# Kernel tuning notes

Hardware: AMD Instinct MI355X
Metric: run time of the kernel (lower is better)

The kernel has to match this reference:

```python
import jax, jax.numpy as jnp
import numpy as np

N_NODES = 32768
N_GRAPHS = 16
N_PER = N_NODES // N_GRAPHS  # 2048 nodes per graph
N_EDGES = 262144
D = 128      # node_state_dim
DE = 64      # edge_state_dim
H = 256      # edge hidden / message dim (= 2*D, required by matching prop)
NH = 256     # node MLP hidden


def _mlp2(x, W1, b1, W2, b2):
    # Linear -> ReLU -> Linear (torch nn.Linear convention: y = x @ W.T + b)
    return jax.nn.relu(x @ W1.T + b1) @ W2.T + b2


def setup_inputs() -> dict:
    key = jax.random.key(0)
    ks = jax.random.split(key, 16)
    s = 0.1  # edge_net_init_scale-ish small init
    inp = {
        "node_states": jax.random.normal(ks[0], (N_NODES, D), jnp.float32),
        "edge_features": jax.random.normal(ks[1], (N_EDGES, DE), jnp.float32),
        "from_idx": jax.random.randint(ks[2], (N_EDGES,), 0, N_NODES, jnp.int32),
        "to_idx": jax.random.randint(ks[3], (N_EDGES,), 0, N_NODES, jnp.int32),
        "graph_idx": jnp.repeat(jnp.arange(N_GRAPHS, dtype=jnp.int32), N_PER),
        "n_graphs": N_GRAPHS,
        # forward message net: Linear(2D+DE -> H), Linear(H -> H)
        "Wm1": jax.random.normal(ks[4], (H, 2 * D + DE), jnp.float32) * s,
        "bm1": jnp.zeros((H,), jnp.float32),
        "Wm2": jax.random.normal(ks[5], (H, H), jnp.float32) * s,
        "bm2": jnp.zeros((H,), jnp.float32),
        # reverse message net (separate params)
        "Wr1": jax.random.normal(ks[6], (H, 2 * D + DE), jnp.float32) * s,
        "br1": jnp.zeros((H,), jnp.float32),
        "Wr2": jax.random.normal(ks[7], (H, H), jnp.float32) * s,
        "br2": jnp.zeros((H,), jnp.float32),
        # node update MLP: Linear(4D -> NH), Linear(NH -> D)
        "Wn1": jax.random.normal(ks[8], (NH, 4 * D), jnp.float32) * s,
        "bn1": jnp.zeros((NH,), jnp.float32),
        "Wn2": jax.random.normal(ks[9], (D, NH), jnp.float32) * s,
        "bn2": jnp.zeros((D,), jnp.float32),
    }
    return inp


def _forward(node_states, edge_features, from_idx, to_idx, n_graphs,
             Wm1, bm1, Wm2, bm2, Wr1, br1, Wr2, br2, Wn1, bn1, Wn2, bn2):
    n = node_states.shape[0]
    fs = node_states[from_idx]   # [E, D] gather
    ts = node_states[to_idx]     # [E, D]
    # forward direction: messages -> scatter-add into to_idx
    m_fwd = _mlp2(jnp.concatenate([fs, ts, edge_features], -1), Wm1, bm1, Wm2, bm2)
    agg = jax.ops.segment_sum(m_fwd, to_idx, num_segments=n)
    # reverse direction: swap endpoints, scatter-add into from_idx
    m_rev = _mlp2(jnp.concatenate([ts, fs, edge_features], -1), Wr1, br1, Wr2, br2)
    agg = agg + jax.ops.segment_sum(m_rev, from_idx, num_segments=n)

    # cross-graph dual-softmax attention over (i, i+1) graph pairs.
    # graph_idx is contiguous equal-size blocks -> reshape partitioning.
    n_per = n // n_graphs
    d = node_states.reshape(n_graphs // 2, 2, n_per, -1)
    x, y = d[:, 0], d[:, 1]                      # [P, Np, D] each
    a = jnp.einsum('pid,pjd->pij', x, y)         # dotproduct similarity
    a_x = jax.nn.softmax(a, axis=2)              # softmax over y per x-row
    a_y = jax.nn.softmax(a, axis=1)              # softmax over x per y-col
    attn_x = jnp.einsum('pij,pjd->pid', a_x, y)  # [P, Np, D]
    attn_y = jnp.einsum('pij,pid->pjd', a_y, x)  # [P, Np, D]
    cross = jnp.stack([attn_x, attn_y], axis=1).reshape(n, -1)

    attention_input = node_states - cross
    node_inputs = jnp.concatenate([agg, attention_input, node_states], -1)  # [N, 4D]
    mlp_out = _mlp2(node_inputs, Wn1, bn1, Wn2, bn2)
    return node_states + mlp_out  # residual update


def reference(node_states, edge_features, from_idx, to_idx, graph_idx, n_graphs,
              Wm1, bm1, Wm2, bm2, Wr1, br1, Wr2, br2, Wn1, bn1, Wn2, bn2):
    return _forward(node_states, edge_features, from_idx, to_idx, int(n_graphs),
                    Wm1, bm1, Wm2, bm2, Wr1, br1, Wr2, br2, Wn1, bn1, Wn2, bn2)
```

## Files before the change

kernel.cpp:

```cpp
#include <hip/hip_runtime.h>


typedef __bf16 bf16_t;
typedef __bf16 bf16x8 __attribute__((ext_vector_type(8)));
typedef __bf16 bf16x4 __attribute__((ext_vector_type(4)));
typedef float  f32x4  __attribute__((ext_vector_type(4)));

#define MFMA16(a,b,c) __builtin_amdgcn_mfma_f32_16x16x32_bf16((a),(b),(c),0,0,0)

constexpr int NNODES = 32768;
constexpr int NEDGES = 262144;
constexpr int DD = 128;
constexpr int HH = 256;

__device__ __forceinline__ bf16x8 cvt8(f32x4 a, f32x4 b){
  bf16x8 r;
  r[0]=(bf16_t)a[0]; r[1]=(bf16_t)a[1]; r[2]=(bf16_t)a[2]; r[3]=(bf16_t)a[3];
  r[4]=(bf16_t)b[0]; r[5]=(bf16_t)b[1]; r[6]=(bf16_t)b[2]; r[7]=(bf16_t)b[3];
  return r;
}

__global__ void cvt_wp_kernel(const float* __restrict__ Wm1, const float* __restrict__ Wr1,
                              bf16_t* __restrict__ wp){
  int idx = (blockIdx.x*256 + threadIdx.x)*4;
  int n = idx >> 7, k = idx & 127;
  const float* W = (n < 512) ? Wm1 : Wr1;
  int row = n & 255;
  int colbase = ((n >> 8) & 1) * 128;
  f32x4 v = *(const f32x4*)(W + (size_t)row*320 + colbase + k);
  bf16x4 o; o[0]=(bf16_t)v[0]; o[1]=(bf16_t)v[1]; o[2]=(bf16_t)v[2]; o[3]=(bf16_t)v[3];
  *(bf16x4*)(wp + idx) = o;
}

__global__ void pack_wc_kernel(const float* __restrict__ Wm1, const float* __restrict__ Wr1,
                               bf16_t* __restrict__ wc){
  int g = blockIdx.x*256 + threadIdx.x;
  int part = g >> 11, gg = g & 2047;
  int tile = gg >> 6, lane = gg & 63;
  int kc = tile >> 4, nt = tile & 15;
  int lr = lane & 15, lk = lane >> 4;
  const float* W = part ? Wr1 : Wm1;
  int row = nt*16 + lr;
  int col = 256 + kc*32 + lk*8;
  f32x4 v0 = *(const f32x4*)(W + (size_t)row*320 + col);
  f32x4 v1 = *(const f32x4*)(W + (size_t)row*320 + col + 4);
  *(bf16x8*)(wc + (size_t)g*8) = cvt8(v0,v1);
}

__global__ void pack_wn2_kernel(const float* __restrict__ Wn2, bf16_t* __restrict__ out){
  int g = blockIdx.x*256 + threadIdx.x;
  int tile = g >> 6, lane = g & 63;
  int kc = tile >> 3, nt = tile & 7;
  int lr = lane & 15, lk = lane >> 4;
  int row = nt*16 + lr;
  int col = kc*32 + lk*8;
  f32x4 v0 = *(const f32x4*)(Wn2 + (size_t)row*256 + col);
  f32x4 v1 = *(const f32x4*)(Wn2 + (size_t)row*256 + col + 4);
  *(bf16x8*)(out + (size_t)g*8) = cvt8(v0,v1);
}

__global__ void hist_kernel(const int* __restrict__ to_idx, const int* __restrict__ from_idx,
                            int* __restrict__ cnt_to, int* __restrict__ cnt_from){
  int e = blockIdx.x*256 + threadIdx.x;
  if (e < NEDGES){
    atomicAdd(&cnt_to[to_idx[e]], 1);
    atomicAdd(&cnt_from[from_idx[e]], 1);
  }
}

__global__ void scan_kernel(int* __restrict__ cnt, int* __restrict__ start){
  __shared__ int sums[1024];
  const int t = threadIdx.x;
  int local[32]; int s = 0;
  #pragma unroll
  for (int j=0;j<32;j++){ local[j] = cnt[t*32+j]; s += local[j]; }
  sums[t] = s; __syncthreads();
  #pragma unroll
  for (int d=1; d<1024; d<<=1){
    int v = (t>=d) ? sums[t-d] : 0;
    __syncthreads();
    sums[t] += v;
    __syncthreads();
  }
  int off = sums[t] - s;
  #pragma unroll
  for (int j=0;j<32;j++){
    start[t*32+j] = off;
    cnt[t*32+j]   = off;
    off += local[j];
  }
  if (t == 1023) start[32768] = sums[1023];
}

__global__ void place_kernel(const int* __restrict__ to_idx, const int* __restrict__ from_idx,
                             int* __restrict__ cur_to, int* __restrict__ cur_from,
                             int* __restrict__ eid_to, int* __restrict__ eid_from,
                             int* __restrict__ rowv_to, int* __restrict__ rowv_from){
  int e = blockIdx.x*256 + threadIdx.x;
  if (e < NEDGES){
    int vt = to_idx[e];
    int p = atomicAdd(&cur_to[vt], 1);
    eid_to[p] = e;
    rowv_to[p] = vt;
    int vf = from_idx[e];
    int q = atomicAdd(&cur_from[vf], 1);
    eid_from[q] = e;
    rowv_from[q] = vf;
  }
}

__global__ __launch_bounds__(256,3) void proj_kernel(
    const float* __restrict__ ns, const bf16_t* __restrict__ Wp,
    bf16_t* __restrict__ P1, bf16_t* __restrict__ P2)
{
  constexpr int XS = 136;
  constexpr int CS = 264;
  __shared__ bf16_t Xs[64*XS];
  __shared__ bf16_t Cs[64*CS];
  const int tid = threadIdx.x;
  const int rb = blockIdx.x*64;
  const int cb = blockIdx.y;
  #pragma unroll
  for (int it=0; it<8; ++it){
    int c = tid + it*256;
    int row = c >> 5, co = (c & 31)*4;
    f32x4 v = *(const f32x4*)(ns + (size_t)(rb+row)*DD + co);
    bf16x4 o; o[0]=(bf16_t)v[0]; o[1]=(bf16_t)v[1]; o[2]=(bf16_t)v[2]; o[3]=(bf16_t)v[3];
    *(bf16x4*)&Xs[row*XS + co] = o;
  }
  __syncthreads();
  const int lane = tid & 63, wave = tid >> 6, lr = lane & 15, lk = lane >> 4;
  const bf16_t* Wb = Wp + (size_t)cb*256*128;
  f32x4 acc[16];
  #pragma unroll
  for (int nt=0;nt<16;nt++) acc[nt] = (f32x4){0.f,0.f,0.f,0.f};
  #pragma unroll
  for (int kc=0;kc<4;kc++){
    bf16x8 a = *(const bf16x8*)&Xs[(wave*16 + lr)*XS + kc*32 + lk*8];
    #pragma unroll
    for (int nt=0;nt<16;nt++){
      bf16x8 b = *(const bf16x8*)&Wb[(size_t)(nt*16 + lr)*128 + kc*32 + lk*8];
      acc[nt] = MFMA16(a,b,acc[nt]);
    }
  }
  #pragma unroll
  for (int nt=0;nt<16;nt++)
    #pragma unroll
    for (int r=0;r<4;r++)
      Cs[(wave*16 + lk*4 + r)*CS + nt*16 + lr] = (bf16_t)acc[nt][r];
  __syncthreads();
  bf16_t* P = cb ? P2 : P1;
  #pragma unroll
  for (int it=0; it<8; ++it){
    int c = tid + it*256;
    int row = c >> 5, co = (c & 31)*8;
    *(bf16x8*)&P[(size_t)(rb+row)*HH + co] = *(const bf16x8*)&Cs[row*CS + co];
  }
}

__global__ __launch_bounds__(256,4) void edge_agg_kernel(
    const float* __restrict__ ef, const bf16_t* __restrict__ Wc,
    const int* __restrict__ eid, const int* __restrict__ oth,
    const int* __restrict__ rowv, const int* __restrict__ start,
    const bf16_t* __restrict__ P1, const bf16_t* __restrict__ P2,
    const float* __restrict__ b1,
    float* __restrict__ partial, bf16_t* __restrict__ aggh)
{
  constexpr int CS = 264;
  __shared__ bf16_t Cs[64*CS];
  __shared__ int es[64], os[64], vs[64];
  const int tid = threadIdx.x;
  const int rb = blockIdx.x*64;
  if (tid < 64){
    int e = eid[rb + tid];
    es[tid] = e;
    os[tid] = oth[e];
    vs[tid] = rowv[rb + tid];
  }
  __syncthreads();

  const int lane = tid & 63, wave = tid >> 6, lr = lane & 15, lk = lane >> 4;
  {
    const float* arow = ef + (size_t)es[wave*16 + lr]*64;
    bf16x8 a0, a1;
    {
      f32x4 v0 = *(const f32x4*)(arow + lk*8);
      f32x4 v1 = *(const f32x4*)(arow + lk*8 + 4);
      a0 = cvt8(v0,v1);
      f32x4 w0 = *(const f32x4*)(arow + 32 + lk*8);
      f32x4 w1 = *(const f32x4*)(arow + 32 + lk*8 + 4);
      a1 = cvt8(w0,w1);
    }
    #pragma unroll
    for (int p=0;p<2;p++){
      f32x4 acc[8];
      #pragma unroll
      for (int nt=0;nt<8;nt++) acc[nt] = (f32x4){0.f,0.f,0.f,0.f};
      #pragma unroll
      for (int nt=0;nt<8;nt++){
        bf16x8 b0 = *(const bf16x8*)&Wc[(size_t)((0*16 + p*8 + nt)*64 + lane)*8];
        acc[nt] = MFMA16(a0,b0,acc[nt]);
        bf16x8 b1v = *(const bf16x8*)&Wc[(size_t)((1*16 + p*8 + nt)*64 + lane)*8];
        acc[nt] = MFMA16(a1,b1v,acc[nt]);
      }
      #pragma unroll
      for (int nt=0;nt<8;nt++)
        #pragma unroll
        for (int r=0;r<4;r++)
          Cs[(wave*16 + lk*4 + r)*CS + (p*8+nt)*16 + lr] = (bf16_t)acc[nt][r];
    }
  }
  __syncthreads();

  const int c8 = (tid & 31) * 8;
  const int rbase = (tid >> 5) * 8;
  {
    f32x4 b1a = *(const f32x4*)(b1 + c8);
    f32x4 b1b = *(const f32x4*)(b1 + c8 + 4);
    #pragma unroll
    for (int j=0;j<8;j++){
      const int row = rbase + j;
      bf16x8 cs = *(const bf16x8*)&Cs[row*CS + c8];
      bf16x8 p1 = *(const bf16x8*)&P1[(size_t)os[row]*HH + c8];
      bf16x8 p2 = *(const bf16x8*)&P2[(size_t)vs[row]*HH + c8];
      bf16x8 o;
      #pragma unroll
      for (int k=0;k<4;k++){
        o[k]   = (bf16_t)fmaxf((float)cs[k]   + (float)p1[k]   + (float)p2[k]   + b1a[k], 0.f);
        o[4+k] = (bf16_t)fmaxf((float)cs[4+k] + (float)p1[4+k] + (float)p2[4+k] + b1b[k], 0.f);
      }
      *(bf16x8*)&Cs[row*CS + c8] = o;
    }
  }
  __syncthreads();

  const int c = tid;
  float runsum = 0.f;
  int curv = vs[0];
  for (int row=0; row<64; ++row){
    const int v = vs[row];
    if (v != curv){
      const int s0 = start[curv], s1 = start[curv+1];
      if (s0 >= rb && s1 <= rb+64)
        aggh[(size_t)curv*HH + c] = (bf16_t)runsum;
      else
        partial[((size_t)curv*2 + (s0 >= rb ? 0 : 1))*HH + c] = runsum;
      runsum = 0.f; curv = v;
    }
    runsum += (float)Cs[row*CS + c];
  }
  {
    const int s0 = start[curv], s1 = start[curv+1];
    if (s0 >= rb && s1 <= rb+64)
      aggh[(size_t)curv*HH + c] = (bf16_t)runsum;
    else
      partial[((size_t)curv*2 + (s0 >= rb ? 0 : 1))*HH + c] = runsum;
  }
}

__global__ __launch_bounds__(256) void combine_kernel(
    const float* __restrict__ partial, const int* __restrict__ start,
    bf16_t* __restrict__ aggh)
{
  const int tid = threadIdx.x;
  const int v = blockIdx.x*8 + (tid>>5);
  const int c0 = (tid & 31)*8;
  const int s0 = start[v], s1 = start[v+1];
  if (s1 == s0){
    bf16x8 z;
    #pragma unroll
    for (int j=0;j<8;j++) z[j] = (bf16_t)0.f;
    *(bf16x8*)&aggh[(size_t)v*HH + c0] = z;
  } else if ((s0>>6) != ((s1-1)>>6)){
    const float* p0 = partial + ((size_t)v*2    )*HH + c0;
    const float* p1 = partial + ((size_t)v*2 + 1)*HH + c0;
    f32x4 a0 = *(const f32x4*)p0;
    f32x4 a1 = *(const f32x4*)(p0+4);
    f32x4 c1 = *(const f32x4*)p1;
    f32x4 c2 = *(const f32x4*)(p1+4);
    bf16x8 o;
    #pragma unroll
    for (int j=0;j<4;j++){ o[j]=(bf16_t)(a0[j]+c1[j]); o[4+j]=(bf16_t)(a1[j]+c2[j]); }
    *(bf16x8*)&aggh[(size_t)v*HH + c0] = o;
  }
}

__global__ __launch_bounds__(256) void w2t_kernel(const float* __restrict__ Wm2, const float* __restrict__ Wr2,
                                                  bf16_t* __restrict__ wm2T, bf16_t* __restrict__ wr2T){
  __shared__ bf16_t t[64][72];
  const int bi = (blockIdx.x & 3)*64;
  const int bj = ((blockIdx.x>>2) & 3)*64;
  const int m  = blockIdx.x >> 4;
  const float* W = m ? Wr2 : Wm2;
  bf16_t* WT = m ? wr2T : wm2T;
  const int tid = threadIdx.x;
  #pragma unroll
  for (int it=0; it<16; ++it){
    int c = tid + it*256;
    int r = c >> 6, co = c & 63;
    t[r][co] = (bf16_t)W[(size_t)(bi+r)*256 + bj + co];
  }
  __syncthreads();
  #pragma unroll
  for (int it=0; it<16; ++it){
    int c = tid + it*256;
    int r = c >> 6, co = c & 63;
    WT[(size_t)(bj+r)*256 + bi + co] = t[co][r];
  }
}

__global__ __launch_bounds__(256,2) void wcat_gemm_kernel(
    const float* __restrict__ Wn1, const bf16_t* __restrict__ wm2T, const bf16_t* __restrict__ wr2T,
    bf16_t* __restrict__ wcat)
{
  constexpr int XS = 264, CS = 264;
  __shared__ bf16_t Xs[64*XS];
  __shared__ bf16_t Cs[64*CS];
  const int tid = threadIdx.x;
  const int rb = blockIdx.x*64;
  const int cb = blockIdx.y;
  const bf16_t* BT = cb ? wr2T : wm2T;
  #pragma unroll
  for (int it=0; it<16; ++it){
    int c = tid + it*256;
    int row = c >> 6, co = (c & 63)*4;
    f32x4 v = *(const f32x4*)(Wn1 + (size_t)(rb+row)*512 + co);
    bf16x4 o; o[0]=(bf16_t)v[0]; o[1]=(bf16_t)v[1]; o[2]=(bf16_t)v[2]; o[3]=(bf16_t)v[3];
    *(bf16x4*)&Xs[row*XS + co] = o;
  }
  __syncthreads();
  const int lane = tid & 63, wave = tid >> 6, lr = lane & 15, lk = lane >> 4;
  f32x4 acc[16];
  #pragma unroll
  for (int nt=0;nt<16;nt++) acc[nt] = (f32x4){0.f,0.f,0.f,0.f};
  #pragma unroll
  for (int kc=0;kc<8;kc++){
    bf16x8 a = *(const bf16x8*)&Xs[(wave*16 + lr)*XS + kc*32 + lk*8];
    #pragma unroll
    for (int nt=0;nt<16;nt++){
      bf16x8 b = *(const bf16x8*)&BT[(size_t)(nt*16 + lr)*256 + kc*32 + lk*8];
      acc[nt] = MFMA16(a,b,acc[nt]);
    }
  }
  #pragma unroll
  for (int nt=0;nt<16;nt++)
    #pragma unroll
    for (int r=0;r<4;r++)
      Cs[(wave*16 + lk*4 + r)*CS + nt*16 + lr] = (bf16_t)acc[nt][r];
  __syncthreads();
  const int nt_base = rb >> 4;
  #pragma unroll
  for (int it=0; it<8; ++it){
    int g = tid + it*256;
    int tile = g >> 6, lane2 = g & 63;
    int kc_l = tile >> 2, nt_l = tile & 3;
    int lr2 = lane2 & 15, lk2 = lane2 >> 4;
    bf16x8 v = *(const bf16x8*)&Cs[(nt_l*16 + lr2)*CS + kc_l*32 + lk2*8];
    *(bf16x8*)&wcat[(size_t)(((cb*8 + kc_l)*16 + nt_base + nt_l)*64 + lane2)*8] = v;
  }
}

__global__ void wcat_copy_kernel(const float* __restrict__ Wn1, bf16_t* __restrict__ wcat){
  int g = blockIdx.x*256 + threadIdx.x;
  int tile = g >> 6, lane = g & 63;
  int kc = tile >> 4, nt = tile & 15;
  int lr = lane & 15, lk = lane >> 4;
  int row = nt*16 + lr;
  int col = 256 + kc*32 + lk*8;
  f32x4 v0 = *(const f32x4*)(Wn1 + (size_t)row*512 + col);
  f32x4 v1 = *(const f32x4*)(Wn1 + (size_t)row*512 + col + 4);
  *(bf16x8*)&wcat[(size_t)(((16 + kc)*16 + nt)*64 + lane)*8] = cvt8(v0,v1);
}

__global__ __launch_bounds__(256) void uw_kernel(const float* __restrict__ Wn1,
    const float* __restrict__ bm2, const float* __restrict__ br2,
    float* __restrict__ u, float* __restrict__ w){
  const int n = threadIdx.x;
  float su=0.f, sw=0.f;
  for (int j=0;j<256;j+=4){
    f32x4 wv = *(const f32x4*)(Wn1 + (size_t)n*512 + j);
    f32x4 bu = *(const f32x4*)(bm2 + j);
    f32x4 bw = *(const f32x4*)(br2 + j);
    #pragma unroll
    for (int q=0;q<4;q++){ su += wv[q]*bu[q]; sw += wv[q]*bw[q]; }
  }
  u[n]=su; w[n]=sw;
}

__global__ __launch_bounds__(256) void nst_kernel(const float* __restrict__ ns,
                                                  bf16_t* __restrict__ nsT,
                                                  bf16_t* __restrict__ nsB){
  constexpr int XS2 = 136;
  __shared__ bf16_t Xs[64*XS2];
  const int tid = threadIdx.x;
  const int nb = blockIdx.x*64;
  #pragma unroll
  for (int it=0; it<8; ++it){
    int c = tid + it*256;
    int rowl = c >> 5, co = (c & 31)*4;
    f32x4 v = *(const f32x4*)(ns + (size_t)(nb+rowl)*DD + co);
    bf16x4 o; o[0]=(bf16_t)v[0]; o[1]=(bf16_t)v[1]; o[2]=(bf16_t)v[2]; o[3]=(bf16_t)v[3];
    *(bf16x4*)&Xs[rowl*XS2 + co] = o;
    *(bf16x4*)&nsB[(size_t)(nb+rowl)*DD + co] = o;
  }
  __syncthreads();
  const int sb = nb >> 11;
  const int jb = nb & 2047;
  bf16_t* outp = nsT + (size_t)sb*DD*2048 + jb;
  #pragma unroll
  for (int it=0; it<4; ++it){
    int c = tid + it*256;
    int d = c >> 3, g8 = (c & 7)*8;
    bf16x8 o;
    #pragma unroll
    for (int k=0;k<8;k++){
      int s64 = g8 + k;
      int t32 = s64 >> 5, s = s64 & 31;
      int m = (s & 1) ? (16 + (s>>1)) : (s>>1);
      o[k] = Xs[(t32*32 + m)*XS2 + d];
    }
    *(bf16x8*)(outp + (size_t)d*2048 + g8) = o;
  }
}

__global__ __launch_bounds__(256,3) void attn_kernel(
    const bf16_t* __restrict__ nsB, const bf16_t* __restrict__ nsT,
    float* __restrict__ Opart, float* __restrict__ lpart)
{
  constexpr int KS = 136;
  constexpr int VS = 40;
  constexpr int PS = 40;
  __shared__ bf16_t Ks[2][32*KS];
  __shared__ bf16_t Vt[2][128*VS];
  __shared__ bf16_t Ps[64*PS];
  const int tid = threadIdx.x;
  const int lane = tid & 63, wave = tid >> 6, lr = lane & 15, lk = lane >> 4;
  const int bx = blockIdx.x;
  const int qt = bx & 31, side = (bx>>5)&1, p = (bx>>6)&7, kvh = bx>>9;
  const size_t qbase = (size_t)p*4096 + (size_t)side*2048 + (size_t)qt*64;
  const int sbkv = p*2 + (side^1);
  const bf16_t* Kv = nsB + ((size_t)p*4096 + (size_t)(side^1)*2048)*DD + (size_t)kvh*32*32*DD;
  const bf16_t* Vp = nsT + (size_t)sbkv*DD*2048 + (size_t)kvh*32*32;

  bf16x8 qf[4];
  {
    const bf16_t* qrow = nsB + (qbase + wave*16 + lr)*DD;
    #pragma unroll
    for (int kc=0;kc<4;kc++) qf[kc] = *(const bf16x8*)(qrow + kc*32 + lk*8);
  }
  float ls[4] = {0.f,0.f,0.f,0.f};
  f32x4 acco[8];
  #pragma unroll
  for (int nt=0;nt<8;nt++) acco[nt]=(f32x4){0.f,0.f,0.f,0.f};

  const int krow0 = tid>>4,        kcol = (tid&15)*8;
  const int vd0   = tid>>2,        vsl  = (tid&3)*8;
  bf16x8 kreg0, kreg1, vreg0, vreg1;

  auto load_tile = [&](int t){
    const bf16_t* kp = Kv + (size_t)t*32*DD;
    kreg0 = *(const bf16x8*)(kp + (size_t)krow0*DD + kcol);
    kreg1 = *(const bf16x8*)(kp + (size_t)(krow0+16)*DD + kcol);
    const bf16_t* vp = Vp + t*32;
    vreg0 = *(const bf16x8*)(vp + (size_t)vd0*2048 + vsl);
    vreg1 = *(const bf16x8*)(vp + (size_t)(vd0+64)*2048 + vsl);
  };
  auto store_tile = [&](int b){
    *(bf16x8*)&Ks[b][krow0*KS + kcol]      = kreg0;
    *(bf16x8*)&Ks[b][(krow0+16)*KS + kcol] = kreg1;
    *(bf16x8*)&Vt[b][vd0*VS + vsl]         = vreg0;
    *(bf16x8*)&Vt[b][(vd0+64)*VS + vsl]    = vreg1;
  };

  load_tile(0);
  store_tile(0);
  load_tile(1);
  __syncthreads();
  int cur = 0;
  for (int t=0; t<32; ++t){
    if (t+1 < 32){
      store_tile(cur^1);
      if (t+2 < 32) load_tile(t+2);
    }
    f32x4 s0 = (f32x4){0.f,0.f,0.f,0.f}, s1 = (f32x4){0.f,0.f,0.f,0.f};
    #pragma unroll
    for (int kc=0;kc<4;kc++){
      bf16x8 b0 = *(const bf16x8*)&Ks[cur][lr*KS      + kc*32 + lk*8];
      bf16x8 b1 = *(const bf16x8*)&Ks[cur][(16+lr)*KS + kc*32 + lk*8];
      s0 = MFMA16(qf[kc], b0, s0);
      s1 = MFMA16(qf[kc], b1, s1);
    }
    #pragma unroll
    for (int r=0;r<4;r++){
      float p0 = __expf(s0[r] - 40.f);
      float p1 = __expf(s1[r] - 40.f);
      ls[r] += p0 + p1;
      union { bf16_t h[2]; unsigned u; } pk;
      pk.h[0] = (bf16_t)p0; pk.h[1] = (bf16_t)p1;
      *(unsigned*)&Ps[(wave*16 + lk*4 + r)*PS + 2*lr] = pk.u;
    }
    asm volatile("s_waitcnt lgkmcnt(0)" ::: "memory");
    __builtin_amdgcn_sched_barrier(0);
    bf16x8 pa = *(const bf16x8*)&Ps[(wave*16 + lr)*PS + lk*8];
    #pragma unroll
    for (int nt=0;nt<8;nt++){
      bf16x8 vb = *(const bf16x8*)&Vt[cur][(nt*16+lr)*VS + lk*8];
      acco[nt] = MFMA16(pa, vb, acco[nt]);
    }
    __syncthreads();
    cur ^= 1;
  }
  #pragma unroll
  for (int r=0;r<4;r++){
    float v = ls[r];
    v += __shfl_xor(v,1); v += __shfl_xor(v,2);
    v += __shfl_xor(v,4); v += __shfl_xor(v,8);
    ls[r] = v;
  }
  float* Op = Opart + (size_t)kvh*NNODES*DD;
  #pragma unroll
  for (int r=0;r<4;r++){
    const size_t row = qbase + wave*16 + lk*4 + r;
    if (lr == 0) lpart[(size_t)kvh*NNODES + row] = ls[r];
    #pragma unroll
    for (int nt=0;nt<8;nt++)
      Op[row*DD + nt*16 + lr] = acco[nt][r];
  }
}

__global__ __launch_bounds__(256) void attn_combine_kernel(
    const float* __restrict__ ns, const float* __restrict__ Opart,
    const float* __restrict__ lpart, bf16_t* __restrict__ attnB)
{
  const int tid = threadIdx.x;
  const int row = blockIdx.x*16 + (tid >> 4);
  const int c0 = (tid & 15)*8;
  const float inv = 1.f/(lpart[row] + lpart[NNODES + row]);
  const float* o0 = Opart + (size_t)row*DD + c0;
  const float* o1 = Opart + (size_t)NNODES*DD + (size_t)row*DD + c0;
  const float* nr = ns + (size_t)row*DD + c0;
  f32x4 a0 = *(const f32x4*)o0,      a1 = *(const f32x4*)(o0+4);
  f32x4 b0 = *(const f32x4*)o1,      b1 = *(const f32x4*)(o1+4);
  f32x4 n0 = *(const f32x4*)nr,      n1 = *(const f32x4*)(nr+4);
  bf16x8 o;
  #pragma unroll
  for (int j=0;j<4;j++){
    o[j]   = (bf16_t)(n0[j] - (a0[j]+b0[j])*inv);
    o[4+j] = (bf16_t)(n1[j] - (a1[j]+b1[j])*inv);
  }
  *(bf16x8*)&attnB[(size_t)row*DD + c0] = o;
}

__global__ __launch_bounds__(256,2) void node_mlp_kernel(
    const bf16_t* __restrict__ agghf, const bf16_t* __restrict__ agghr,
    const bf16_t* __restrict__ attnB, const bf16_t* __restrict__ nsB,
    const float* __restrict__ ns,
    const bf16_t* __restrict__ wcat, const float* __restrict__ bn1,
    const float* __restrict__ uvec, const float* __restrict__ wvec,
    const int* __restrict__ start_to, const int* __restrict__ start_from,
    const bf16_t* __restrict__ Wn2b, const float* __restrict__ bn2,
    float* __restrict__ out)
{
  __shared__ __align__(16) bf16_t As[32*768];
  bf16_t* Hs = As;
  const int tid = threadIdx.x;
  const int lane = tid & 63, wave = tid >> 6, lr = lane & 15, lk = lane >> 4;
  const int rb = blockIdx.x*32;

  bf16x8 stg[12];
  int dsta[12];
  #pragma unroll
  for (int it=0; it<12; ++it){
    const int db = it*4096 + tid*16;
    const int row = db / 1536;
    const int within = db - row*1536;
    const size_t node = (size_t)(rb + row);
    const char* s0 = (const char*)agghf + (node<<9) + within;
    const char* s1 = (const char*)agghr + (node<<9) + (within-512);
    const char* s2 = (const char*)attnB + (node<<8) + (within-1024);
    const char* s3 = (const char*)nsB   + (node<<8) + (within-1280);
    const char* src = within < 512 ? s0 : (within < 1024 ? s1 : (within < 1280 ? s2 : s3));
    stg[it] = *(const bf16x8*)src;
    dsta[it] = row*1536 + (within ^ ((row & 7) << 4));
  }
  #pragma unroll
  for (int it=0; it<12; ++it)
    *(bf16x8*)((char*)As + dsta[it]) = stg[it];
  __syncthreads();

  const int cg = wave >> 1;
  const int colbase = cg * 128;
  const int arow = (wave & 1)*16 + lr;
  const unsigned abase = (unsigned)arow * 1536u;
  const unsigned asw = ((unsigned)(arow & 7)) << 4;
  f32x4 acc[8];
  #pragma unroll
  for (int nt=0;nt<8;nt++) acc[nt] = (f32x4){0.f,0.f,0.f,0.f};
  #pragma unroll
  for (int kc=0; kc<24; ++kc){
    const unsigned y = (unsigned)(kc*64 + lk*16);
    bf16x8 a = *(const bf16x8*)((const char*)As + abase + (y ^ asw));
    #pragma unroll
    for (int nt=0;nt<8;nt++){
      bf16x8 b = *(const bf16x8*)&wcat[(size_t)((kc*16 + cg*8 + nt)*64 + lane)*8];
      acc[nt] = MFMA16(a,b,acc[nt]);
    }
  }
  __syncthreads();

  const int r0 = rb + (wave&1)*16 + lk*4;
  float dt[4], df[4];
  #pragma unroll
  for (int r=0;r<4;r++){
    dt[r] = (float)(start_to[r0+r+1]   - start_to[r0+r]);
    df[r] = (float)(start_from[r0+r+1] - start_from[r0+r]);
  }
  #pragma unroll
  for (int nt=0;nt<8;nt++){
    const int col = colbase + nt*16 + lr;
    const float bias = bn1[col];
    const float uu = uvec[col], ww = wvec[col];
    #pragma unroll
    for (int r=0;r<4;r++){
      float v = acc[nt][r] + bias + dt[r]*uu + df[r]*ww;
      v = v > 0.f ? v : 0.f;
      Hs[((wave&1)*16 + lk*4 + r)*264 + col] = (bf16_t)v;
    }
  }
  __syncthreads();

  const int cb2 = cg * 64;
  f32x4 acc2[4];
  #pragma unroll
  for (int nt=0;nt<4;nt++) acc2[nt] = (f32x4){0.f,0.f,0.f,0.f};
  #pragma unroll
  for (int kc=0;kc<8;kc++){
    bf16x8 a = *(const bf16x8*)&Hs[((wave&1)*16 + lr)*264 + kc*32 + lk*8];
    #pragma unroll
    for (int nt=0;nt<4;nt++){
      bf16x8 b = *(const bf16x8*)&Wn2b[(size_t)((kc*8 + cg*4 + nt)*64 + lane)*8];
      acc2[nt] = MFMA16(a,b,acc2[nt]);
    }
  }
  #pragma unroll
  for (int nt=0;nt<4;nt++){
    const int col = cb2 + nt*16 + lr;
    const float bias = bn2[col];
    #pragma unroll
    for (int r=0;r<4;r++){
      const size_t rr = (size_t)(r0 + r);
      out[rr*DD + col] = acc2[nt][r] + bias + ns[rr*DD + col];
    }
  }
}

extern "C" void kernel_launch(void* const* d_in, const int* in_sizes, int n_in,
                              void* d_out, int out_size, void* d_ws, size_t ws_size,
                              hipStream_t stream) {
  const float* ns  = (const float*)d_in[0];
  const float* ef  = (const float*)d_in[1];
  const int* from_idx = (const int*)d_in[2];
  const int* to_idx   = (const int*)d_in[3];
  const float* Wm1 = (const float*)d_in[6];  const float* bm1 = (const float*)d_in[7];
  const float* Wm2 = (const float*)d_in[8];  const float* bm2 = (const float*)d_in[9];
  const float* Wr1 = (const float*)d_in[10]; const float* br1 = (const float*)d_in[11];
  const float* Wr2 = (const float*)d_in[12]; const float* br2 = (const float*)d_in[13];
  const float* Wn1 = (const float*)d_in[14]; const float* bn1 = (const float*)d_in[15];
  const float* Wn2 = (const float*)d_in[16]; const float* bn2 = (const float*)d_in[17];

  char* ws = (char*)d_ws;
  float*  partial  = (float*)(ws);
  int*    rowv_to   = (int*)(ws + 67108864);
  int*    rowv_from = (int*)(ws + 68157440);
  bf16_t* P1t    = (bf16_t*)(ws + 134217728);
  bf16_t* P2t    = (bf16_t*)(ws + 150994944);
  bf16_t* aggh_f = (bf16_t*)(ws + 167772160);
  bf16_t* aggh_r = (bf16_t*)(ws + 184549376);
  bf16_t* wpb  = (bf16_t*)(ws + 201326592);
  bf16_t* wcb  = (bf16_t*)(ws + 201588736);
  bf16_t* wn2b = (bf16_t*)(ws + 201654272);
  int* cur_to     = (int*)(ws + 202244096);
  int* cur_from   = (int*)(ws + 202375168);
  int* start_to   = (int*)(ws + 202506240);
  int* start_from = (int*)(ws + 202637320);
  int* eid_to     = (int*)(ws + 202768400);
  int* eid_from   = (int*)(ws + 203816976);
  bf16_t* attnB = (bf16_t*)(ws);
  bf16_t* nsB   = (bf16_t*)(ws + 33554432);
  bf16_t* nsT   = (bf16_t*)(ws + 41943040);
  bf16_t* wm2T  = (bf16_t*)(ws + 50331648);
  bf16_t* wr2T  = (bf16_t*)(ws + 50462720);
  bf16_t* wcat  = (bf16_t*)(ws + 50593792);
  float*  uvec  = (float*) (ws + 50987008);
  float*  wvec  = (float*) (ws + 50988032);
  float*  Opart = (float*) (ws + 69206016);
  float*  lpart = (float*) (ws + 102760448);

  hipMemsetAsync(cur_to, 0, 2*NNODES*sizeof(int), stream);

  cvt_wp_kernel<<<128, 256, 0, stream>>>(Wm1, Wr1, wpb);
  pack_wc_kernel<<<16, 256, 0, stream>>>(Wm1, Wr1, wcb);
  pack_wn2_kernel<<<16, 256, 0, stream>>>(Wn2, wn2b);

  hist_kernel<<<NEDGES/256, 256, 0, stream>>>(to_idx, from_idx, cur_to, cur_from);
  scan_kernel<<<1, 1024, 0, stream>>>(cur_to, start_to);
  scan_kernel<<<1, 1024, 0, stream>>>(cur_from, start_from);
  place_kernel<<<NEDGES/256, 256, 0, stream>>>(to_idx, from_idx, cur_to, cur_from,
      eid_to, eid_from, rowv_to, rowv_from);

  proj_kernel<<<dim3(NNODES/64, 2), 256, 0, stream>>>(ns, wpb, P1t, P2t);
  edge_agg_kernel<<<NEDGES/64, 256, 0, stream>>>(ef, wcb, eid_to, from_idx,
      rowv_to, start_to, P1t, P2t, bm1, partial, aggh_f);
  combine_kernel<<<NNODES/8, 256, 0, stream>>>(partial, start_to, aggh_f);

  proj_kernel<<<dim3(NNODES/64, 2), 256, 0, stream>>>(ns, wpb + 512*128, P1t, P2t);
  edge_agg_kernel<<<NEDGES/64, 256, 0, stream>>>(ef, wcb + 256*64, eid_from, to_idx,
      rowv_from, start_from, P1t, P2t, br1, partial, aggh_r);
  combine_kernel<<<NNODES/8, 256, 0, stream>>>(partial, start_from, aggh_r);

  nst_kernel<<<NNODES/64, 256, 0, stream>>>(ns, nsT, nsB);
  w2t_kernel<<<32, 256, 0, stream>>>(Wm2, Wr2, wm2T, wr2T);
  wcat_gemm_kernel<<<dim3(4,2), 256, 0, stream>>>(Wn1, wm2T, wr2T, wcat);
  wcat_copy_kernel<<<32, 256, 0, stream>>>(Wn1, wcat);
  uw_kernel<<<1, 256, 0, stream>>>(Wn1, bm2, br2, uvec, wvec);

  attn_kernel<<<1024, 256, 0, stream>>>(nsB, nsT, Opart, lpart);
  attn_combine_kernel<<<NNODES/16, 256, 0, stream>>>(ns, Opart, lpart, attnB);

  node_mlp_kernel<<<NNODES/32, 256, 0, stream>>>(aggh_f, aggh_r, attnB, nsB, ns,
      wcat, bn1, uvec, wvec, start_to, start_from, wn2b, bn2, (float*)d_out);
}
```

Before: 452.8 us.

## Merge forward/reverse edge passes and fuse small prep kernels into fewer launches

Fuses the three weight-pack kernels, the two scans, the two directions of proj/edge_agg/combine, and the w2t/uw/wcat_copy kernels into single launches using block-index dispatch. It also moves the first-layer bias into the P2 projection and stores split-segment partials in bf16 instead of fp32. The goals are fewer kernel launches, more concurrent blocks for the edge work, and less partial-sum traffic. The cost is extra workspace for separate forward and reverse P buffers, plus a small precision loss from the bf16 partials and the earlier bias rounding.

```diff
diff --git a/kernel.cpp b/kernel.cpp
--- a/kernel.cpp
+++ b/kernel.cpp
@@ -20,43 +20,44 @@
   return r;
 }
 
-__global__ void cvt_wp_kernel(const float* __restrict__ Wm1, const float* __restrict__ Wr1,
-                              bf16_t* __restrict__ wp){
-  int idx = (blockIdx.x*256 + threadIdx.x)*4;
-  int n = idx >> 7, k = idx & 127;
-  const float* W = (n < 512) ? Wm1 : Wr1;
-  int row = n & 255;
-  int colbase = ((n >> 8) & 1) * 128;
-  f32x4 v = *(const f32x4*)(W + (size_t)row*320 + colbase + k);
-  bf16x4 o; o[0]=(bf16_t)v[0]; o[1]=(bf16_t)v[1]; o[2]=(bf16_t)v[2]; o[3]=(bf16_t)v[3];
-  *(bf16x4*)(wp + idx) = o;
-}
-
-__global__ void pack_wc_kernel(const float* __restrict__ Wm1, const float* __restrict__ Wr1,
-                               bf16_t* __restrict__ wc){
-  int g = blockIdx.x*256 + threadIdx.x;
-  int part = g >> 11, gg = g & 2047;
-  int tile = gg >> 6, lane = gg & 63;
-  int kc = tile >> 4, nt = tile & 15;
-  int lr = lane & 15, lk = lane >> 4;
-  const float* W = part ? Wr1 : Wm1;
-  int row = nt*16 + lr;
-  int col = 256 + kc*32 + lk*8;
-  f32x4 v0 = *(const f32x4*)(W + (size_t)row*320 + col);
-  f32x4 v1 = *(const f32x4*)(W + (size_t)row*320 + col + 4);
-  *(bf16x8*)(wc + (size_t)g*8) = cvt8(v0,v1);
-}
-
-__global__ void pack_wn2_kernel(const float* __restrict__ Wn2, bf16_t* __restrict__ out){
-  int g = blockIdx.x*256 + threadIdx.x;
-  int tile = g >> 6, lane = g & 63;
-  int kc = tile >> 3, nt = tile & 7;
-  int lr = lane & 15, lk = lane >> 4;
-  int row = nt*16 + lr;
-  int col = kc*32 + lk*8;
-  f32x4 v0 = *(const f32x4*)(Wn2 + (size_t)row*256 + col);
-  f32x4 v1 = *(const f32x4*)(Wn2 + (size_t)row*256 + col + 4);
-  *(bf16x8*)(out + (size_t)g*8) = cvt8(v0,v1);
+__global__ void pack_weights_kernel(const float* __restrict__ Wm1, const float* __restrict__ Wr1,
+                                    const float* __restrict__ Wn2,
+                                    bf16_t* __restrict__ wp, bf16_t* __restrict__ wc,
+                                    bf16_t* __restrict__ wn2){
+  const int bx = blockIdx.x;
+  const int tid = threadIdx.x;
+  if (bx < 128){
+    int idx = (bx*256 + tid)*4;
+    int n = idx >> 7, k = idx & 127;
+    const float* W = (n < 512) ? Wm1 : Wr1;
+    int row = n & 255;
+    int colbase = ((n >> 8) & 1) * 128;
+    f32x4 v = *(const f32x4*)(W + (size_t)row*320 + colbase + k);
+    bf16x4 o; o[0]=(bf16_t)v[0]; o[1]=(bf16_t)v[1]; o[2]=(bf16_t)v[2]; o[3]=(bf16_t)v[3];
+    *(bf16x4*)(wp + idx) = o;
+  } else if (bx < 144){
+    int g = (bx-128)*256 + tid;
+    int part = g >> 11, gg = g & 2047;
+    int tile = gg >> 6, lane = gg & 63;
+    int kc = tile >> 4, nt = tile & 15;
+    int lr = lane & 15, lk = lane >> 4;
+    const float* W = part ? Wr1 : Wm1;
+    int row = nt*16 + lr;
+    int col = 256 + kc*32 + lk*8;
+    f32x4 v0 = *(const f32x4*)(W + (size_t)row*320 + col);
+    f32x4 v1 = *(const f32x4*)(W + (size_t)row*320 + col + 4);
+    *(bf16x8*)(wc + (size_t)g*8) = cvt8(v0,v1);
+  } else {
+    int g = (bx-144)*256 + tid;
+    int tile = g >> 6, lane = g & 63;
+    int kc = tile >> 3, nt = tile & 7;
+    int lr = lane & 15, lk = lane >> 4;
+    int row = nt*16 + lr;
+    int col = kc*32 + lk*8;
+    f32x4 v0 = *(const f32x4*)(Wn2 + (size_t)row*256 + col);
+    f32x4 v1 = *(const f32x4*)(Wn2 + (size_t)row*256 + col + 4);
+    *(bf16x8*)(wn2 + (size_t)g*8) = cvt8(v0,v1);
+  }
 }
 
 __global__ void hist_kernel(const int* __restrict__ to_idx, const int* __restrict__ from_idx,
@@ -68,7 +69,10 @@
   }
 }
 
-__global__ void scan_kernel(int* __restrict__ cnt, int* __restrict__ start){
+__global__ void scan_kernel(int* __restrict__ cnt_to, int* __restrict__ cnt_from,
+                            int* __restrict__ start_to, int* __restrict__ start_from){
+  int* cnt   = blockIdx.x ? cnt_from : cnt_to;
+  int* start = blockIdx.x ? start_from : start_to;
   __shared__ int sums[1024];
   const int t = threadIdx.x;
   int local[32]; int s = 0;
@@ -111,7 +115,9 @@
 
 __global__ __launch_bounds__(256,3) void proj_kernel(
     const float* __restrict__ ns, const bf16_t* __restrict__ Wp,
-    bf16_t* __restrict__ P1, bf16_t* __restrict__ P2)
+    const float* __restrict__ bm1, const float* __restrict__ br1,
+    bf16_t* __restrict__ P1f, bf16_t* __restrict__ P2f,
+    bf16_t* __restrict__ P1r, bf16_t* __restrict__ P2r)
 {
   constexpr int XS = 136;
   constexpr int CS = 264;
@@ -120,6 +126,8 @@
   const int tid = threadIdx.x;
   const int rb = blockIdx.x*64;
   const int cb = blockIdx.y;
+  const int dir = blockIdx.z;
+  const float* bvec = dir ? br1 : bm1;
   #pragma unroll
   for (int it=0; it<8; ++it){
     int c = tid + it*256;
@@ -130,7 +138,7 @@
   }
   __syncthreads();
   const int lane = tid & 63, wave = tid >> 6, lr = lane & 15, lk = lane >> 4;
-  const bf16_t* Wb = Wp + (size_t)cb*256*128;
+  const bf16_t* Wb = Wp + (size_t)(dir*2 + cb)*32768;
   f32x4 acc[16];
   #pragma unroll
   for (int nt=0;nt<16;nt++) acc[nt] = (f32x4){0.f,0.f,0.f,0.f};
@@ -144,12 +152,14 @@
     }
   }
   #pragma unroll
-  for (int nt=0;nt<16;nt++)
+  for (int nt=0;nt<16;nt++){
+    const float bias = cb ? bvec[nt*16 + lr] : 0.f;
     #pragma unroll
     for (int r=0;r<4;r++)
-      Cs[(wave*16 + lk*4 + r)*CS + nt*16 + lr] = (bf16_t)acc[nt][r];
-  __syncthreads();
-  bf16_t* P = cb ? P2 : P1;
+      Cs[(wave*16 + lk*4 + r)*CS + nt*16 + lr] = (bf16_t)(acc[nt][r] + bias);
+  }
+  __syncthreads();
+  bf16_t* P = dir ? (cb ? P2r : P1r) : (cb ? P2f : P1f);
   #pragma unroll
   for (int it=0; it<8; ++it){
     int c = tid + it*256;
@@ -160,17 +170,31 @@
 
 __global__ __launch_bounds__(256,4) void edge_agg_kernel(
     const float* __restrict__ ef, const bf16_t* __restrict__ Wc,
-    const int* __restrict__ eid, const int* __restrict__ oth,
-    const int* __restrict__ rowv, const int* __restrict__ start,
-    const bf16_t* __restrict__ P1, const bf16_t* __restrict__ P2,
-    const float* __restrict__ b1,
-    float* __restrict__ partial, bf16_t* __restrict__ aggh)
+    const int* __restrict__ eid_to, const int* __restrict__ eid_from,
+    const int* __restrict__ from_idx, const int* __restrict__ to_idx,
+    const int* __restrict__ rowv_to, const int* __restrict__ rowv_from,
+    const int* __restrict__ start_to, const int* __restrict__ start_from,
+    const bf16_t* __restrict__ P1f, const bf16_t* __restrict__ P2f,
+    const bf16_t* __restrict__ P1r, const bf16_t* __restrict__ P2r,
+    bf16_t* __restrict__ partial_f, bf16_t* __restrict__ partial_r,
+    bf16_t* __restrict__ aggh_f, bf16_t* __restrict__ aggh_r)
 {
   constexpr int CS = 264;
   __shared__ bf16_t Cs[64*CS];
   __shared__ int es[64], os[64], vs[64];
   const int tid = threadIdx.x;
-  const int rb = blockIdx.x*64;
+  const int dir = blockIdx.x >> 12;
+  const int rb = (blockIdx.x & 4095)*64;
+  const int* eid  = dir ? eid_from  : eid_to;
+  const int* oth  = dir ? to_idx    : from_idx;
+  const int* rowv = dir ? rowv_from : rowv_to;
+  const int* start= dir ? start_from: start_to;
+  const bf16_t* P1 = dir ? P1r : P1f;
+  const bf16_t* P2 = dir ? P2r : P2f;
+  bf16_t* partial  = dir ? partial_r : partial_f;
+  bf16_t* aggh     = dir ? aggh_r : aggh_f;
+  const bf16_t* Wcd = Wc + (size_t)dir*16384;
+
   if (tid < 64){
     int e = eid[rb + tid];
     es[tid] = e;
@@ -198,9 +222,9 @@
       for (int nt=0;nt<8;nt++) acc[nt] = (f32x4){0.f,0.f,0.f,0.f};
       #pragma unroll
       for (int nt=0;nt<8;nt++){
-        bf16x8 b0 = *(const bf16x8*)&Wc[(size_t)((0*16 + p*8 + nt)*64 + lane)*8];
+        bf16x8 b0 = *(const bf16x8*)&Wcd[(size_t)((0*16 + p*8 + nt)*64 + lane)*8];
         acc[nt] = MFMA16(a0,b0,acc[nt]);
-        bf16x8 b1v = *(const bf16x8*)&Wc[(size_t)((1*16 + p*8 + nt)*64 + lane)*8];
+        bf16x8 b1v = *(const bf16x8*)&Wcd[(size_t)((1*16 + p*8 + nt)*64 + lane)*8];
         acc[nt] = MFMA16(a1,b1v,acc[nt]);
       }
       #pragma unroll
@@ -215,8 +239,6 @@
   const int c8 = (tid & 31) * 8;
   const int rbase = (tid >> 5) * 8;
   {
-    f32x4 b1a = *(const f32x4*)(b1 + c8);
-    f32x4 b1b = *(const f32x4*)(b1 + c8 + 4);
     #pragma unroll
     for (int j=0;j<8;j++){
       const int row = rbase + j;
@@ -225,10 +247,8 @@
       bf16x8 p2 = *(const bf16x8*)&P2[(size_t)vs[row]*HH + c8];
       bf16x8 o;
       #pragma unroll
-      for (int k=0;k<4;k++){
-        o[k]   = (bf16_t)fmaxf((float)cs[k]   + (float)p1[k]   + (float)p2[k]   + b1a[k], 0.f);
-        o[4+k] = (bf16_t)fmaxf((float)cs[4+k] + (float)p1[4+k] + (float)p2[4+k] + b1b[k], 0.f);
-      }
+      for (int k=0;k<8;k++)
+        o[k] = (bf16_t)fmaxf((float)cs[k] + (float)p1[k] + (float)p2[k], 0.f);
       *(bf16x8*)&Cs[row*CS + c8] = o;
     }
   }
@@ -244,7 +264,7 @@
       if (s0 >= rb && s1 <= rb+64)
         aggh[(size_t)curv*HH + c] = (bf16_t)runsum;
       else
-        partial[((size_t)curv*2 + (s0 >= rb ? 0 : 1))*HH + c] = runsum;
+        partial[((size_t)curv*2 + (s0 >= rb ? 0 : 1))*HH + c] = (bf16_t)runsum;
       runsum = 0.f; curv = v;
     }
     runsum += (float)Cs[row*CS + c];
@@ -254,14 +274,19 @@
     if (s0 >= rb && s1 <= rb+64)
       aggh[(size_t)curv*HH + c] = (bf16_t)runsum;
     else
-      partial[((size_t)curv*2 + (s0 >= rb ? 0 : 1))*HH + c] = runsum;
+      partial[((size_t)curv*2 + (s0 >= rb ? 0 : 1))*HH + c] = (bf16_t)runsum;
   }
 }
 
 __global__ __launch_bounds__(256) void combine_kernel(
-    const float* __restrict__ partial, const int* __restrict__ start,
-    bf16_t* __restrict__ aggh)
+    const bf16_t* __restrict__ partial_f, const bf16_t* __restrict__ partial_r,
+    const int* __restrict__ start_to, const int* __restrict__ start_from,
+    bf16_t* __restrict__ aggh_f, bf16_t* __restrict__ aggh_r)
 {
+  const int dir = blockIdx.y;
+  const bf16_t* partial = dir ? partial_r : partial_f;
+  const int* start = dir ? start_from : start_to;
+  bf16_t* aggh = dir ? aggh_r : aggh_f;
   const int tid = threadIdx.x;
   const int v = blockIdx.x*8 + (tid>>5);
   const int c0 = (tid & 31)*8;
@@ -272,21 +297,33 @@
     for (int j=0;j<8;j++) z[j] = (bf16_t)0.f;
     *(bf16x8*)&aggh[(size_t)v*HH + c0] = z;
   } else if ((s0>>6) != ((s1-1)>>6)){
-    const float* p0 = partial + ((size_t)v*2    )*HH + c0;
-    const float* p1 = partial + ((size_t)v*2 + 1)*HH + c0;
-    f32x4 a0 = *(const f32x4*)p0;
-    f32x4 a1 = *(const f32x4*)(p0+4);
-    f32x4 c1 = *(const f32x4*)p1;
-    f32x4 c2 = *(const f32x4*)(p1+4);
+    bf16x8 a = *(const bf16x8*)&partial[((size_t)v*2    )*HH + c0];
+    bf16x8 b = *(const bf16x8*)&partial[((size_t)v*2 + 1)*HH + c0];
     bf16x8 o;
     #pragma unroll
-    for (int j=0;j<4;j++){ o[j]=(bf16_t)(a0[j]+c1[j]); o[4+j]=(bf16_t)(a1[j]+c2[j]); }
+    for (int j=0;j<8;j++) o[j] = (bf16_t)((float)a[j] + (float)b[j]);
     *(bf16x8*)&aggh[(size_t)v*HH + c0] = o;
   }
 }
 
-__global__ __launch_bounds__(256) void w2t_kernel(const float* __restrict__ Wm2, const float* __restrict__ Wr2,
-                                                  bf16_t* __restrict__ wm2T, bf16_t* __restrict__ wr2T){
+__global__ __launch_bounds__(256) void w2t_uw_kernel(const float* __restrict__ Wm2, const float* __restrict__ Wr2,
+                                                     bf16_t* __restrict__ wm2T, bf16_t* __restrict__ wr2T,
+                                                     const float* __restrict__ Wn1,
+                                                     const float* __restrict__ bm2, const float* __restrict__ br2,
+                                                     float* __restrict__ u, float* __restrict__ w){
+  if (blockIdx.x == 32){
+    const int n = threadIdx.x;
+    float su=0.f, sw=0.f;
+    for (int j=0;j<256;j+=4){
+      f32x4 wv = *(const f32x4*)(Wn1 + (size_t)n*512 + j);
+      f32x4 bu = *(const f32x4*)(bm2 + j);
+      f32x4 bw = *(const f32x4*)(br2 + j);
+      #pragma unroll
+      for (int q=0;q<4;q++){ su += wv[q]*bu[q]; sw += wv[q]*bw[q]; }
+    }
+    u[n]=su; w[n]=sw;
+    return;
+  }
   __shared__ bf16_t t[64][72];
   const int bi = (blockIdx.x & 3)*64;
   const int bj = ((blockIdx.x>>2) & 3)*64;
@@ -314,11 +351,26 @@
     bf16_t* __restrict__ wcat)
 {
   constexpr int XS = 264, CS = 264;
+  const int tid = threadIdx.x;
+  const int cb = blockIdx.y;
+  if (cb == 2){
+    #pragma unroll
+    for (int it=0; it<8; ++it){
+      int g = blockIdx.x*2048 + it*256 + tid;
+      int tile = g >> 6, lane = g & 63;
+      int kc = tile >> 4, nt = tile & 15;
+      int lr = lane & 15, lk = lane >> 4;
+      int row = nt*16 + lr;
+      int col = 256 + kc*32 + lk*8;
+      f32x4 v0 = *(const f32x4*)(Wn1 + (size_t)row*512 + col);
+      f32x4 v1 = *(const f32x4*)(Wn1 + (size_t)row*512 + col + 4);
+      *(bf16x8*)&wcat[(size_t)(((16 + kc)*16 + nt)*64 + lane)*8] = cvt8(v0,v1);
+    }
+    return;
+  }
   __shared__ bf16_t Xs[64*XS];
   __shared__ bf16_t Cs[64*CS];
-  const int tid = threadIdx.x;
   const int rb = blockIdx.x*64;
-  const int cb = blockIdx.y;
   const bf16_t* BT = cb ? wr2T : wm2T;
   #pragma unroll
   for (int it=0; it<16; ++it){
@@ -358,33 +410,6 @@
     bf16x8 v = *(const bf16x8*)&Cs[(nt_l*16 + lr2)*CS + kc_l*32 + lk2*8];
     *(bf16x8*)&wcat[(size_t)(((cb*8 + kc_l)*16 + nt_base + nt_l)*64 + lane2)*8] = v;
   }
-}
-
-__global__ void wcat_copy_kernel(const float* __restrict__ Wn1, bf16_t* __restrict__ wcat){
-  int g = blockIdx.x*256 + threadIdx.x;
-  int tile = g >> 6, lane = g & 63;
-  int kc = tile >> 4, nt = tile & 15;
-  int lr = lane & 15, lk = lane >> 4;
-  int row = nt*16 + lr;
-  int col = 256 + kc*32 + lk*8;
-  f32x4 v0 = *(const f32x4*)(Wn1 + (size_t)row*512 + col);
-  f32x4 v1 = *(const f32x4*)(Wn1 + (size_t)row*512 + col + 4);
-  *(bf16x8*)&wcat[(size_t)(((16 + kc)*16 + nt)*64 + lane)*8] = cvt8(v0,v1);
-}
-
-__global__ __launch_bounds__(256) void uw_kernel(const float* __restrict__ Wn1,
-    const float* __restrict__ bm2, const float* __restrict__ br2,
-    float* __restrict__ u, float* __restrict__ w){
-  const int n = threadIdx.x;
-  float su=0.f, sw=0.f;
-  for (int j=0;j<256;j+=4){
-    f32x4 wv = *(const f32x4*)(Wn1 + (size_t)n*512 + j);
-    f32x4 bu = *(const f32x4*)(bm2 + j);
-    f32x4 bw = *(const f32x4*)(br2 + j);
-    #pragma unroll
-    for (int q=0;q<4;q++){ su += wv[q]*bu[q]; sw += wv[q]*bw[q]; }
-  }
-  u[n]=su; w[n]=sw;
 }
 
 __global__ __launch_bounds__(256) void nst_kernel(const float* __restrict__ ns,
@@ -669,11 +694,14 @@
   const float* Wn2 = (const float*)d_in[16]; const float* bn2 = (const float*)d_in[17];
 
   char* ws = (char*)d_ws;
-  float*  partial  = (float*)(ws);
+  bf16_t* partial_f = (bf16_t*)(ws);
+  bf16_t* partial_r = (bf16_t*)(ws + 33554432);
   int*    rowv_to   = (int*)(ws + 67108864);
   int*    rowv_from = (int*)(ws + 68157440);
-  bf16_t* P1t    = (bf16_t*)(ws + 134217728);
-  bf16_t* P2t    = (bf16_t*)(ws + 150994944);
+  bf16_t* P1r   = (bf16_t*)(ws + 69206016);
+  bf16_t* P2r   = (bf16_t*)(ws + 85983232);
+  bf16_t* P1f   = (bf16_t*)(ws + 134217728);
+  bf16_t* P2f   = (bf16_t*)(ws + 150994944);
   bf16_t* aggh_f = (bf16_t*)(ws + 167772160);
   bf16_t* aggh_r = (bf16_t*)(ws + 184549376);
   bf16_t* wpb  = (bf16_t*)(ws + 201326592);
@@ -698,31 +726,26 @@
 
   hipMemsetAsync(cur_to, 0, 2*NNODES*sizeof(int), stream);
 
-  cvt_wp_kernel<<<128, 256, 0, stream>>>(Wm1, Wr1, wpb);
-  pack_wc_kernel<<<16, 256, 0, stream>>>(Wm1, Wr1, wcb);
-  pack_wn2_kernel<<<16, 256, 0, stream>>>(Wn2, wn2b);
+  pack_weights_kernel<<<160, 256, 0, stream>>>(Wm1, Wr1, Wn2, wpb, wcb, wn2b);
 
   hist_kernel<<<NEDGES/256, 256, 0, stream>>>(to_idx, from_idx, cur_to, cur_from);
-  scan_kernel<<<1, 1024, 0, stream>>>(cur_to, start_to);
-  scan_kernel<<<1, 1024, 0, stream>>>(cur_from, start_from);
+  scan_kernel<<<2, 1024, 0, stream>>>(cur_to, cur_from, start_to, start_from);
   place_kernel<<<NEDGES/256, 256, 0, stream>>>(to_idx, from_idx, cur_to, cur_from,
       eid_to, eid_from, rowv_to, rowv_from);
 
-  proj_kernel<<<dim3(NNODES/64, 2), 256, 0, stream>>>(ns, wpb, P1t, P2t);
-  edge_agg_kernel<<<NEDGES/64, 256, 0, stream>>>(ef, wcb, eid_to, from_idx,
-      rowv_to, start_to, P1t, P2t, bm1, partial, aggh_f);
-  combine_kernel<<<NNODES/8, 256, 0, stream>>>(partial, start_to, aggh_f);
-
-  proj_kernel<<<dim3(NNODES/64, 2), 256, 0, stream>>>(ns, wpb + 512*128, P1t, P2t);
-  edge_agg_kernel<<<NEDGES/64, 256, 0, stream>>>(ef, wcb + 256*64, eid_from, to_idx,
-      rowv_from, start_from, P1t, P2t, br1, partial, aggh_r);
-  combine_kernel<<<NNODES/8, 256, 0, stream>>>(partial, start_from, aggh_r);
+  proj_kernel<<<dim3(NNODES/64, 2, 2), 256, 0, stream>>>(ns, wpb, bm1, br1,
+      P1f, P2f, P1r, P2r);
+
+  edge_agg_kernel<<<2*NEDGES/64, 256, 0, stream>>>(ef, wcb,
+      eid_to, eid_from, from_idx, to_idx, rowv_to, rowv_from, start_to, start_from,
+      P1f, P2f, P1r, P2r, partial_f, partial_r, aggh_f, aggh_r);
+
+  combine_kernel<<<dim3(NNODES/8, 2), 256, 0, stream>>>(partial_f, partial_r,
+      start_to, start_from, aggh_f, aggh_r);
 
   nst_kernel<<<NNODES/64, 256, 0, stream>>>(ns, nsT, nsB);
-  w2t_kernel<<<32, 256, 0, stream>>>(Wm2, Wr2, wm2T, wr2T);
-  wcat_gemm_kernel<<<dim3(4,2), 256, 0, stream>>>(Wn1, wm2T, wr2T, wcat);
-  wcat_copy_kernel<<<32, 256, 0, stream>>>(Wn1, wcat);
-  uw_kernel<<<1, 256, 0, stream>>>(Wn1, bm2, br2, uvec, wvec);
+  w2t_uw_kernel<<<33, 256, 0, stream>>>(Wm2, Wr2, wm2T, wr2T, Wn1, bm2, br2, uvec, wvec);
+  wcat_gemm_kernel<<<dim3(4,3), 256, 0, stream>>>(Wn1, wm2T, wr2T, wcat);
 
   attn_kernel<<<1024, 256, 0, stream>>>(nsB, nsT, Opart, lpart);
   attn_combine_kernel<<<NNODES/16, 256, 0, stream>>>(ns, Opart, lpart, attnB);
```

Result: faster. 412.4 us (-8.9%).
